# Kernel optimization log

Hardware: AMD Instinct MI355X
Metric: run time of the kernel (lower is better)

The kernel has to match this reference:

```python
import jax, jax.numpy as jnp
import numpy as np

N_ENT = 100000
N_USR = 30000
N_TOT = N_ENT + N_USR
N_REL = 32
D = 64
E = 500000
INTER = 500000
N_LAYERS = 2
SLOPE = 0.01  # torch nn.LeakyReLU default negative slope


def _seg_softmax(logits, seg, n):
    # sparse softmax over rows (segments)
    m = jax.ops.segment_max(logits, seg, num_segments=n)
    ex = jnp.exp(logits - m[seg])
    den = jax.ops.segment_sum(ex, seg, num_segments=n)
    return ex / den[seg]


def setup_inputs() -> dict:
    key = jax.random.key(0)
    k = jax.random.split(key, 14)
    all_embed = jax.random.normal(k[0], (N_TOT, D), jnp.float32) * 0.1
    rel_embed = jax.random.normal(k[1], (N_REL, D), jnp.float32) * 0.1
    Wk_w = jax.random.normal(k[2], (D, 2 * D), jnp.float32) / np.sqrt(2 * D)
    Wk_b = jnp.zeros((D,), jnp.float32)
    Wa_w = jax.random.normal(k[3], (D, D), jnp.float32) / np.sqrt(D)
    Wb_w = jax.random.normal(k[4], (D, D), jnp.float32) / np.sqrt(D)
    # KG edge lists (head entity, tail entity, relation)
    h_list = jnp.sort(jax.random.randint(k[5], (E,), 0, N_ENT))
    t_list = jax.random.randint(k[6], (E,), 0, N_ENT)
    r_list = jax.random.randint(k[7], (E,), 0, N_REL)
    # bipartite interaction matrix A_in (symmetric, items rows first then users)
    u = jax.random.randint(k[8], (INTER,), 0, N_USR)
    it = jax.random.randint(k[9], (INTER,), 0, N_ENT)
    a_row = jnp.concatenate([it, N_ENT + u])
    a_col = jnp.concatenate([N_ENT + u, it])
    a_vals = jax.random.uniform(k[10], (2 * INTER,), jnp.float32) * 0.01
    # calc_score ids: user ids are offset by n_entities in the concatenated table
    user_ids = N_ENT + jax.random.randint(k[11], (1024,), 0, N_USR)
    item_ids = jax.random.randint(k[12], (2048,), 0, N_ENT)
    return dict(all_embed=all_embed, rel_embed=rel_embed, Wk_w=Wk_w, Wk_b=Wk_b,
                Wa_w=Wa_w, Wb_w=Wb_w, a_vals=a_vals, user_ids=user_ids,
                item_ids=item_ids, h_list=h_list, t_list=t_list, r_list=r_list,
                a_row=a_row, a_col=a_col)


def _get_embeddings(all_embed, rel_embed, Wk_w, Wk_b, Wa_w, Wb_w, a_vals,
                    h_list, t_list, r_list, a_row, a_col):
    e_ent = all_embed[:N_ENT]
    e_usr = all_embed[N_ENT:]
    user_list = [e_usr]
    item_list = [e_ent]
    e_items_dual = e_ent
    e_users_curr = e_usr
    e_ent_curr = e_ent
    r_e = rel_embed[r_list]  # (E, D) -- constant across layers
    for _ in range(N_LAYERS):
        # --- KG attention (Eq. 2): gather + concat + linear + dot + leakyrelu ---
        h_e = e_ent_curr[h_list]            # (E, D)
        t_e = e_ent_curr[t_list]            # (E, D)
        cat = jnp.concatenate([t_e, h_e], axis=1)   # (E, 2D)
        trans = cat @ Wk_w.T + Wk_b                 # (E, D)
        logits = jnp.sum(trans * r_e, axis=1)       # (E,)
        vals = jnp.where(logits >= 0, logits, SLOPE * logits)
        alpha = _seg_softmax(vals, h_list, N_ENT)   # row-wise sparse softmax
        # --- KG aggregation (Eq. 1): spmm ---
        e_items_kg = jax.ops.segment_sum(alpha[:, None] * t_e, h_list,
                                         num_segments=N_ENT)
        # --- IG aggregation (Eq. 3 & 6): spmm with A_in ---
        ig_in = jnp.concatenate([e_items_dual, e_users_curr], axis=0)  # (N_TOT, D)
        ig_out = jax.ops.segment_sum(a_vals[:, None] * ig_in[a_col], a_row,
                                     num_segments=N_TOT)
        e_items_collab = ig_out[:N_ENT]
        e_users_new = ig_out[N_ENT:]
        # --- fusion gate (Eq. 4, 5) ---
        g = jax.nn.sigmoid(e_items_kg @ Wa_w.T + e_items_collab @ Wb_w.T)
        e_items_dual = g * e_items_kg + (1.0 - g) * e_items_collab
        item_list.append(e_items_collab)
        user_list.append(e_users_new)
        e_users_curr = e_users_new
        e_ent_curr = e_items_kg
    item_final = sum(item_list)
    user_final = sum(user_list)
    return jnp.concatenate([item_final, user_final], axis=0)


def reference(all_embed, rel_embed, Wk_w, Wk_b, Wa_w, Wb_w, a_vals,
              user_ids, item_ids, h_list, t_list, r_list, a_row, a_col):
    all_final = _get_embeddings(all_embed, rel_embed, Wk_w, Wk_b, Wa_w, Wb_w,
                                a_vals, h_list, t_list, r_list, a_row, a_col)
    user_e = all_final[user_ids]   # (Bu, D)
    item_e = all_final[item_ids]   # (Bi, D)
    return user_e @ item_e.T       # (Bu, Bi)
```

## Files before the change

### kernel.cpp

```cpp
#include <hip/hip_runtime.h>

#define N_ENT 100000
#define N_USR 30000
#define N_TOTN 130000
#define N_RELC 32
#define DIM 64
#define NEDGE 500000
#define INTER 500000
#define SLOPE 0.01f
#define CPT_NB 127
#define FILL_NB 489
#define MARK_NB 489
#define ATT_NB 1024
#define SP_NB 1024
#define RSTR 64
#define KGOFF_NB 1954
#define FR_TR 17
#define FR_R2 19
#define FR_KG 31
#define FR_MK 1985
#define FR_NB 2474

typedef unsigned char u8;
typedef unsigned int u32;
typedef unsigned long long u64;

__device__ __forceinline__ float grp_sum16(float v){
  v += __shfl_xor(v, 8, 64);
  v += __shfl_xor(v, 4, 64);
  v += __shfl_xor(v, 2, 64);
  v += __shfl_xor(v, 1, 64);
  return v;
}

__global__ void __launch_bounds__(256) k_front(
    const float* __restrict__ rel, const float* __restrict__ Wk,
    const float* __restrict__ Wkb, float* __restrict__ m, float* __restrict__ b,
    const float* __restrict__ Wa, const float* __restrict__ Wb,
    float* __restrict__ wat, float* __restrict__ wbt,
    const int* __restrict__ user_ids, const int* __restrict__ item_ids,
    u8* __restrict__ r2_item, u8* __restrict__ r2_user,
    const int* __restrict__ h_list, int* __restrict__ off,
    const int4* __restrict__ a_row4, const int4* __restrict__ a_col4,
    u8* __restrict__ need_d, u8* __restrict__ need_u){
  int bid = blockIdx.x;
  int t = threadIdx.x;
  if (bid < FR_TR){
    int idx = bid*256 + t;
    if (idx < N_RELC*128){
      int r = idx >> 7, j = idx & 127;
      float s = 0.f;
      for (int d = 0; d < DIM; ++d) s += rel[r*DIM+d] * Wk[d*128+j];
      m[idx] = s;
    } else if (idx < N_RELC*128 + N_RELC){
      int r = idx - N_RELC*128;
      float s = 0.f;
      for (int d = 0; d < DIM; ++d) s += Wkb[d] * rel[r*DIM+d];
      b[r] = s;
    }
  } else if (bid < FR_R2){
    int base = (bid - FR_TR)*2048;
    for (int i = t; i < 2048; i += 256){
      int idx = base + i;
      int k = idx >> 6, d = idx & 63;
      wat[idx] = Wa[d*64 + k];
      wbt[idx] = Wb[d*64 + k];
    }
  } else if (bid < FR_KG){
    int i = (bid - FR_R2)*256 + t;
    if (i < 1024) r2_user[user_ids[i] - N_ENT] = 1;
    else if (i < 3072) r2_item[item_ids[i - 1024]] = 1;
  } else if (bid < FR_MK){
    int e = (bid - FR_KG)*256 + t;
    if (e <= NEDGE){
      int hc = (e < NEDGE) ? h_list[e] : N_ENT;
      int hp = (e == 0) ? -1 : h_list[e-1];
      for (int s = hp+1; s <= hc; ++s) off[s] = e;
    }
  } else {
    __shared__ u32 bm_item[(N_ENT + 31)/32];
    __shared__ u32 bm_user[(N_USR + 31)/32];
    for (int i = t; i < (N_ENT+31)/32; i += 256) bm_item[i] = 0;
    for (int i = t; i < (N_USR+31)/32; i += 256) bm_user[i] = 0;
    __syncthreads();
    for (int i = t; i < 3072; i += 256){
      if (i < 1024){ int u = user_ids[i] - N_ENT; atomicOr(&bm_user[u>>5], 1u << (u&31)); }
      else { int it = item_ids[i - 1024]; atomicOr(&bm_item[it>>5], 1u << (it&31)); }
    }
    __syncthreads();
    int i = (bid - FR_MK)*256 + t;
    if (i < INTER/4){
      int4 ar = a_row4[i];
      int4 ac = a_col4[i];
      #pragma unroll
      for (int k = 0; k < 4; ++k){
        int it = (&ar.x)[k];
        int uu = (&ac.x)[k] - N_ENT;
        if ((bm_item[it>>5] >> (it&31)) & 1u) need_u[uu] = 1;
        if ((bm_user[uu>>5] >> (uu&31)) & 1u) need_d[it] = 1;
      }
    }
  }
}

__global__ void __launch_bounds__(256) k_buildfill(
    const int* __restrict__ a_row, const int* __restrict__ a_col,
    const float* __restrict__ a_vals,
    const u8* __restrict__ need_d, const u8* __restrict__ need_u,
    const u8* __restrict__ r2_item, const u8* __restrict__ r2_user,
    int* __restrict__ list_gate, int* __restrict__ list_s1,
    int* __restrict__ counters, int* __restrict__ cnt, int2* __restrict__ csr){
  if (blockIdx.x < CPT_NB){
    __shared__ u64 mg_sh[16], ms_sh[16];
    __shared__ int pre_g[16], pre_s[16];
    __shared__ int base_sh[2];
    int t = threadIdx.x;
    int wave = t >> 6, lane = t & 63;
    bool pg[4], ps[4];
    int ibase = blockIdx.x*1024;
    #pragma unroll
    for (int k = 0; k < 4; ++k){
      int i = ibase + k*256 + t;
      bool g = false, s = false;
      if (i < N_TOTN){
        if (i < N_ENT){ g = need_d[i] != 0; s = (!g) && (r2_item[i] != 0); }
        else { int u = i - N_ENT; s = (need_u[u] != 0) || (r2_user[u] != 0); }
      }
      pg[k] = g; ps[k] = s;
      u64 mg = __ballot(g), ms = __ballot(s);
      if (lane == 0){ mg_sh[k*4 + wave] = mg; ms_sh[k*4 + wave] = ms; }
    }
    __syncthreads();
    if (t == 0){
      int sg = 0, ss = 0;
      for (int j = 0; j < 16; ++j){
        pre_g[j] = sg; sg += __popcll(mg_sh[j]);
        pre_s[j] = ss; ss += __popcll(ms_sh[j]);
      }
      base_sh[0] = sg ? atomicAdd(&counters[0], sg) : 0;
      base_sh[1] = ss ? atomicAdd(&counters[1], ss) : 0;
    }
    __syncthreads();
    int bg = base_sh[0], bs = base_sh[1];
    u64 lmask = (1ull << lane) - 1;
    #pragma unroll
    for (int k = 0; k < 4; ++k){
      int i = ibase + k*256 + t;
      if (pg[k]) list_gate[bg + pre_g[k*4+wave] + __popcll(mg_sh[k*4+wave] & lmask)] = i;
      if (ps[k]) list_s1 [bs + pre_s[k*4+wave] + __popcll(ms_sh[k*4+wave] & lmask)] = i;
    }
  } else {
    int i = (blockIdx.x - CPT_NB)*256 + threadIdx.x;
    if (i >= INTER/4) return;
    int4 ar = ((const int4*)a_row)[i];
    int4 ac = ((const int4*)a_col)[i];
    float4 av0 = ((const float4*)a_vals)[i];
    float4 av1 = ((const float4*)(a_vals + INTER))[i];
    #pragma unroll
    for (int k = 0; k < 4; ++k){
      int it = (&ar.x)[k];
      int uc = (&ac.x)[k];
      int uu = uc - N_ENT;
      if (need_d[it] | r2_item[it]){
        int p = atomicAdd(&cnt[it], 1);
        if (p < RSTR) csr[((size_t)it << 6) + p] = make_int2(uc, __float_as_int((&av0.x)[k]));
      }
      if (need_u[uu] | r2_user[uu]){
        int p = atomicAdd(&cnt[uc], 1);
        if (p < RSTR) csr[((size_t)uc << 6) + p] = make_int2(it, __float_as_int((&av1.x)[k]));
      }
    }
  }
}

__global__ void __launch_bounds__(256, 8) k_l1g(const float4* __restrict__ ent4,
    const float4* __restrict__ m4, const float* __restrict__ bvec,
    const float4* __restrict__ wat4, const float4* __restrict__ wbt4,
    const int* __restrict__ off, const int* __restrict__ t_list,
    const int* __restrict__ r_list, const int* __restrict__ list_gate,
    const int* __restrict__ list_s1, const int* __restrict__ counters,
    const int* __restrict__ cnt, const int2* __restrict__ csr,
    float4* __restrict__ collab4, float4* __restrict__ x2_4){
  int t = threadIdx.x;
  int sub = t & 15;
  if (blockIdx.x < ATT_NB){
    int n = counters[0];
    int grp = (blockIdx.x*256 + t) >> 4;
    int ng = (ATT_NB*256) >> 4;
    for (int idx = grp; idx < n; idx += ng){
      int s = list_gate[idx];
      int beg = off[s], end = off[s+1];
      float4 h4 = ent4[(size_t)s*16 + sub];
      float l = 0.f;
      float4 acc = {0.f,0.f,0.f,0.f};
      for (int base = beg; base < end; base += 16){
        int mch = end - base; if (mch > 16) mch = 16;
        int tj = 0, rj = 0;
        if (sub < mch){ tj = t_list[base + sub]; rj = r_list[base + sub]; }
        #pragma unroll 4
        for (int j = 0; j < mch; ++j){
          int ti = __shfl(tj, j, 16);
          int r  = __shfl(rj, j, 16);
          float4 t4 = ent4[(size_t)ti*16 + sub];
          float4 mt = m4[r*32 + sub];
          float4 mh = m4[r*32 + 16 + sub];
          float v = t4.x*mt.x + t4.y*mt.y + t4.z*mt.z + t4.w*mt.w
                  + h4.x*mh.x + h4.y*mh.y + h4.z*mh.z + h4.w*mh.w;
          v = grp_sum16(v) + bvec[r];
          v = (v >= 0.f) ? v : SLOPE * v;
          float w = __expf(v);
          l += w;
          acc.x += w*t4.x; acc.y += w*t4.y; acc.z += w*t4.z; acc.w += w*t4.w;
        }
      }
      float inv = (end > beg) ? 1.f / l : 0.f;
      float4 kg = {acc.x*inv, acc.y*inv, acc.z*inv, acc.w*inv};
      int deg = cnt[s]; if (deg > RSTR) deg = RSTR;
      size_t base0 = (size_t)s << 6;
      float4 cb = {0.f,0.f,0.f,0.f};
      for (int b = 0; b < deg; b += 16){
        int mch = deg - b; if (mch > 16) mch = 16;
        int2 e = make_int2(0, 0);
        if (sub < mch) e = csr[base0 + b + sub];
        #pragma unroll 4
        for (int j = 0; j < mch; ++j){
          int cj = __shfl(e.x, j, 16);
          float vj = __int_as_float(__shfl(e.y, j, 16));
          float4 sv = ent4[(size_t)cj*16 + sub];
          cb.x += vj*sv.x; cb.y += vj*sv.y; cb.z += vj*sv.z; cb.w += vj*sv.w;
        }
      }
      float4 ga = {0.f,0.f,0.f,0.f};
      for (int kk = 0; kk < 16; ++kk){
        float kqx = __shfl(kg.x, kk, 16), kqy = __shfl(kg.y, kk, 16);
        float kqz = __shfl(kg.z, kk, 16), kqw = __shfl(kg.w, kk, 16);
        float cqx = __shfl(cb.x, kk, 16), cqy = __shfl(cb.y, kk, 16);
        float cqz = __shfl(cb.z, kk, 16), cqw = __shfl(cb.w, kk, 16);
        int k0 = kk*4;
        float4 wa0 = wat4[(k0+0)*16 + sub];
        float4 wa1 = wat4[(k0+1)*16 + sub];
        float4 wa2 = wat4[(k0+2)*16 + sub];
        float4 wa3 = wat4[(k0+3)*16 + sub];
        float4 wb0 = wbt4[(k0+0)*16 + sub];
        float4 wb1 = wbt4[(k0+1)*16 + sub];
        float4 wb2 = wbt4[(k0+2)*16 + sub];
        float4 wb3 = wbt4[(k0+3)*16 + sub];
        ga.x += kqx*wa0.x + kqy*wa1.x + kqz*wa2.x + kqw*wa3.x
              + cqx*wb0.x + cqy*wb1.x + cqz*wb2.x + cqw*wb3.x;
        ga.y += kqx*wa0.y + kqy*wa1.y + kqz*wa2.y + kqw*wa3.y
              + cqx*wb0.y + cqy*wb1.y + cqz*wb2.y + cqw*wb3.y;
        ga.z += kqx*wa0.z + kqy*wa1.z + kqz*wa2.z + kqw*wa3.z
              + cqx*wb0.z + cqy*wb1.z + cqz*wb2.z + cqw*wb3.z;
        ga.w += kqx*wa0.w + kqy*wa1.w + kqz*wa2.w + kqw*wa3.w
              + cqx*wb0.w + cqy*wb1.w + cqz*wb2.w + cqw*wb3.w;
      }
      float4 o;
      #pragma unroll
      for (int j = 0; j < 4; ++j){
        float g = 1.f / (1.f + __expf(-(&ga.x)[j]));
        (&o.x)[j] = g*(&kg.x)[j] + (1.f - g)*(&cb.x)[j];
      }
      collab4[(size_t)s*16 + sub] = cb;
      x2_4[(size_t)s*16 + sub] = o;
    }
  } else {
    int n = counters[1];
    int bid = blockIdx.x - ATT_NB;
    int grp = (bid*256 + t) >> 4;
    int ng = (SP_NB*256) >> 4;
    for (int idx = grp; idx < n; idx += ng){
      int i = list_s1[idx];
      int deg = cnt[i]; if (deg > RSTR) deg = RSTR;
      size_t base0 = (size_t)i << 6;
      float4 acc = {0.f,0.f,0.f,0.f};
      for (int b = 0; b < deg; b += 16){
        int mch = deg - b; if (mch > 16) mch = 16;
        int2 e = make_int2(0, 0);
        if (sub < mch) e = csr[base0 + b + sub];
        #pragma unroll 8
        for (int j = 0; j < mch; ++j){
          int cj = __shfl(e.x, j, 16);
          float vj = __int_as_float(__shfl(e.y, j, 16));
          float4 sv = ent4[(size_t)cj*16 + sub];
          acc.x += vj*sv.x; acc.y += vj*sv.y; acc.z += vj*sv.z; acc.w += vj*sv.w;
        }
      }
      if (i < N_ENT) collab4[(size_t)i*16 + sub] = acc;
      else x2_4[(size_t)i*16 + sub] = acc;
    }
  }
}

__global__ void __launch_bounds__(256) k_spmm2g(const int* __restrict__ cnt,
    const int2* __restrict__ csr, const float* __restrict__ x2,
    const float* __restrict__ all_embed, const float* __restrict__ collab1,
    const int* __restrict__ user_ids, const int* __restrict__ item_ids,
    float* __restrict__ user_e, float* __restrict__ item_e){
  int lane = threadIdx.x & 63;
  int g = (blockIdx.x*256 + threadIdx.x) >> 6;
  if (g >= 3072) return;
  int id;
  float b1;
  if (g < 1024){
    id = user_ids[g];
    b1 = x2[(size_t)id*64 + lane];
  } else {
    id = item_ids[g - 1024];
    b1 = collab1[(size_t)id*64 + lane];
  }
  float acc = all_embed[(size_t)id*64 + lane] + b1;
  int deg = cnt[id]; if (deg > RSTR) deg = RSTR;
  size_t base0 = (size_t)id << 6;
  int2 e = make_int2(0, 0);
  if (lane < deg) e = csr[base0 + lane];
  #pragma unroll 8
  for (int j = 0; j < deg; ++j){
    int cj = __shfl(e.x, j, 64);
    float vj = __int_as_float(__shfl(e.y, j, 64));
    acc += vj * x2[(size_t)cj*64 + lane];
  }
  if (g < 1024) user_e[(size_t)g*64 + lane] = acc;
  else item_e[(size_t)(g - 1024)*64 + lane] = acc;
}

__global__ void __launch_bounds__(256) k_out(const float* __restrict__ ue,
    const float* __restrict__ ie, float* __restrict__ out){
  __shared__ float ash[64][65];
  __shared__ float bsh[64][65];
  int row0 = blockIdx.y * 64, col0 = blockIdx.x * 64;
  for (int i = threadIdx.x; i < 64*64; i += 256){
    int r = i >> 6, c = i & 63;
    ash[r][c] = ue[(size_t)(row0 + r)*DIM + c];
    bsh[r][c] = ie[(size_t)(col0 + r)*DIM + c];
  }
  __syncthreads();
  int tx = threadIdx.x & 15, ty = threadIdx.x >> 4;
  int r0 = ty*4, c0 = tx*4;
  float acc[4][4] = {};
  #pragma unroll
  for (int k = 0; k < 64; ++k){
    float a0 = ash[r0][k], a1 = ash[r0+1][k], a2 = ash[r0+2][k], a3 = ash[r0+3][k];
    float b0 = bsh[c0][k], b1 = bsh[c0+1][k], b2 = bsh[c0+2][k], b3 = bsh[c0+3][k];
    acc[0][0] += a0*b0; acc[0][1] += a0*b1; acc[0][2] += a0*b2; acc[0][3] += a0*b3;
    acc[1][0] += a1*b0; acc[1][1] += a1*b1; acc[1][2] += a1*b2; acc[1][3] += a1*b3;
    acc[2][0] += a2*b0; acc[2][1] += a2*b1; acc[2][2] += a2*b2; acc[2][3] += a2*b3;
    acc[3][0] += a3*b0; acc[3][1] += a3*b1; acc[3][2] += a3*b2; acc[3][3] += a3*b3;
  }
  #pragma unroll
  for (int i = 0; i < 4; ++i){
    float4 o = {acc[i][0], acc[i][1], acc[i][2], acc[i][3]};
    *(float4*)&out[(size_t)(row0 + r0 + i)*2048 + col0 + c0] = o;
  }
}

extern "C" void kernel_launch(void* const* d_in, const int* in_sizes, int n_in,
                              void* d_out, int out_size, void* d_ws, size_t ws_size,
                              hipStream_t stream){
  const float* all_embed = (const float*)d_in[0];
  const float* rel_embed = (const float*)d_in[1];
  const float* Wk_w      = (const float*)d_in[2];
  const float* Wk_b      = (const float*)d_in[3];
  const float* Wa_w      = (const float*)d_in[4];
  const float* Wb_w      = (const float*)d_in[5];
  const float* a_vals    = (const float*)d_in[6];
  const int* user_ids   = (const int*)d_in[7];
  const int* item_ids   = (const int*)d_in[8];
  const int* h_list     = (const int*)d_in[9];
  const int* t_list     = (const int*)d_in[10];
  const int* r_list     = (const int*)d_in[11];
  const int* a_row      = (const int*)d_in[12];
  const int* a_col      = (const int*)d_in[13];
  float* out = (float*)d_out;

  char* p = (char*)d_ws;
  auto alloc = [&](size_t bytes)->void*{
    void* r = (void*)p;
    p += (bytes + 255) & ~(size_t)255;
    return r;
  };
  float* m_rel   = (float*)alloc((size_t)N_RELC*128*4);
  float* b_rel   = (float*)alloc((size_t)N_RELC*4);
  float* wat     = (float*)alloc((size_t)64*64*4);
  float* wbt     = (float*)alloc((size_t)64*64*4);
  int*   kg_off  = (int*)  alloc((size_t)(N_ENT+1)*4);
  size_t zbytes = (size_t)N_TOTN*4 + 256 + (2*(size_t)N_ENT + 2*(size_t)N_USR);
  char*  zbase  = (char*)alloc(zbytes);
  int*   cnt      = (int*)zbase;
  int*   counters = (int*)(zbase + (size_t)N_TOTN*4);
  u8*    r2_item  = (u8*)(zbase + (size_t)N_TOTN*4 + 256);
  u8*    r2_user  = r2_item + N_ENT;
  u8*    need_d   = r2_user + N_USR;
  u8*    need_u   = need_d + N_ENT;
  int2*  csr     = (int2*) alloc((size_t)N_TOTN*RSTR*8);
  int*   list_gate = (int*)alloc((size_t)N_ENT*4);
  int*   list_s1   = (int*)alloc((size_t)N_TOTN*4);
  float* collab1 = (float*)alloc((size_t)N_ENT*DIM*4);
  float* x2      = (float*)alloc((size_t)N_TOTN*DIM*4);
  float* user_e  = (float*)alloc((size_t)1024*DIM*4);
  float* item_e  = (float*)alloc((size_t)2048*DIM*4);

  hipMemsetAsync(zbase, 0, zbytes, stream);
  k_front<<<FR_NB, 256, 0, stream>>>(rel_embed, Wk_w, Wk_b, m_rel, b_rel,
      Wa_w, Wb_w, wat, wbt, user_ids, item_ids, r2_item, r2_user,
      h_list, kg_off, (const int4*)a_row, (const int4*)a_col, need_d, need_u);
  k_buildfill<<<CPT_NB + FILL_NB, 256, 0, stream>>>(a_row, a_col, a_vals,
      need_d, need_u, r2_item, r2_user, list_gate, list_s1, counters, cnt, csr);

  k_l1g<<<ATT_NB + SP_NB, 256, 0, stream>>>((const float4*)all_embed,
      (const float4*)m_rel, b_rel, (const float4*)wat, (const float4*)wbt,
      kg_off, t_list, r_list, list_gate, list_s1, counters, cnt, csr,
      (float4*)collab1, (float4*)x2);

  k_spmm2g<<<768, 256, 0, stream>>>(cnt, csr, x2, all_embed, collab1,
      user_ids, item_ids, user_e, item_e);
  dim3 grid_out(2048/64, 1024/64);
  k_out<<<grid_out, 256, 0, stream>>>(user_e, item_e, out);
}
```

Before: 188.8 us.

## Replace static attention/SpMM block split with dynamic atomic work queue

```diff
diff --git a/kernel.cpp b/kernel.cpp
--- a/kernel.cpp
+++ b/kernel.cpp
@@ -10,11 +10,8 @@
 #define SLOPE 0.01f
 #define CPT_NB 127
 #define FILL_NB 489
-#define MARK_NB 489
-#define ATT_NB 1024
-#define SP_NB 1024
 #define RSTR 64
-#define KGOFF_NB 1954
+#define L1G_NB 2048
 #define FR_TR 17
 #define FR_R2 19
 #define FR_KG 31
@@ -178,25 +175,31 @@
     const float4* __restrict__ wat4, const float4* __restrict__ wbt4,
     const int* __restrict__ off, const int* __restrict__ t_list,
     const int* __restrict__ r_list, const int* __restrict__ list_gate,
-    const int* __restrict__ list_s1, const int* __restrict__ counters,
+    const int* __restrict__ list_s1, int* __restrict__ counters,
     const int* __restrict__ cnt, const int2* __restrict__ csr,
     float4* __restrict__ collab4, float4* __restrict__ x2_4){
   int t = threadIdx.x;
   int sub = t & 15;
-  if (blockIdx.x < ATT_NB){
-    int n = counters[0];
-    int grp = (blockIdx.x*256 + t) >> 4;
-    int ng = (ATT_NB*256) >> 4;
-    for (int idx = grp; idx < n; idx += ng){
+  int gig = (t >> 4) & 3;
+  int n0 = counters[0];
+  int ntot = n0 + counters[1];
+  for (;;){
+    int base;
+    if ((t & 63) == 0) base = atomicAdd(&counters[16], 4);
+    base = __shfl(base, (t & 192), 64);
+    if (base >= ntot) break;
+    int idx = base + gig;
+    if (idx >= ntot) continue;
+    if (idx < n0){
       int s = list_gate[idx];
       int beg = off[s], end = off[s+1];
       float4 h4 = ent4[(size_t)s*16 + sub];
       float l = 0.f;
       float4 acc = {0.f,0.f,0.f,0.f};
-      for (int base = beg; base < end; base += 16){
-        int mch = end - base; if (mch > 16) mch = 16;
+      for (int bb = beg; bb < end; bb += 16){
+        int mch = end - bb; if (mch > 16) mch = 16;
         int tj = 0, rj = 0;
-        if (sub < mch){ tj = t_list[base + sub]; rj = r_list[base + sub]; }
+        if (sub < mch){ tj = t_list[bb + sub]; rj = r_list[bb + sub]; }
         #pragma unroll 4
         for (int j = 0; j < mch; ++j){
           int ti = __shfl(tj, j, 16);
@@ -262,14 +265,8 @@
       }
       collab4[(size_t)s*16 + sub] = cb;
       x2_4[(size_t)s*16 + sub] = o;
-    }
-  } else {
-    int n = counters[1];
-    int bid = blockIdx.x - ATT_NB;
-    int grp = (bid*256 + t) >> 4;
-    int ng = (SP_NB*256) >> 4;
-    for (int idx = grp; idx < n; idx += ng){
-      int i = list_s1[idx];
+    } else {
+      int i = list_s1[idx - n0];
       int deg = cnt[i]; if (deg > RSTR) deg = RSTR;
       size_t base0 = (size_t)i << 6;
       float4 acc = {0.f,0.f,0.f,0.f};
@@ -406,7 +403,7 @@
   k_buildfill<<<CPT_NB + FILL_NB, 256, 0, stream>>>(a_row, a_col, a_vals,
       need_d, need_u, r2_item, r2_user, list_gate, list_s1, counters, cnt, csr);
 
-  k_l1g<<<ATT_NB + SP_NB, 256, 0, stream>>>((const float4*)all_embed,
+  k_l1g<<<L1G_NB, 256, 0, stream>>>((const float4*)all_embed,
       (const float4*)m_rel, b_rel, (const float4*)wat, (const float4*)wbt,
       kg_off, t_list, r_list, list_gate, list_s1, counters, cnt, csr,
       (float4*)collab1, (float4*)x2);
```

New measurement: 333.3 us. 1.77x slower.
